# Kernel tuning notes

Measured on AMD Instinct MI355X. Metric: run time of the kernel, lower is better.

## Reference

```python
import jax, jax.numpy as jnp
import numpy as np
from jax import lax

EPS = 1e-5
NUM_HEADS = 8
HEAD_DIM = 64
NUM_DEVICES = 8
MAX_DEV = 3       # max_devices_per_token
TOP_K = 6         # num_experts_per_tok
EBF, DBF, CBF = 0.003, 0.05, 0.02  # aux loss factors


def rms_norm(x, eps=EPS):
    xf = x.astype(jnp.float32)
    var = jnp.mean(jnp.square(xf), axis=-1, keepdims=True)
    return (xf * lax.rsqrt(var + eps)).astype(x.dtype)


def rotate_half(x):
    x1, x2 = jnp.split(x, 2, axis=-1)
    return jnp.concatenate([-x2, x1], axis=-1)


def swiglu(x, wgu, wd):
    gate, up = jnp.split(x @ wgu, 2, axis=-1)
    return (jax.nn.silu(gate) * up) @ wd


def attention(x, w_qkv, w_o, cos, sin):
    B, S, H = x.shape
    qkv = (x @ w_qkv).reshape(B, S, 3 * NUM_HEADS, HEAD_DIM)
    q, k, v = (qkv[:, :, :NUM_HEADS], qkv[:, :, NUM_HEADS:2 * NUM_HEADS],
               qkv[:, :, 2 * NUM_HEADS:])
    c = cos[None, :, None, :]
    s = sin[None, :, None, :]
    q = q * c + rotate_half(q) * s
    k = k * c + rotate_half(k) * s
    scores = jnp.einsum('bqhd,bkhd->bhqk', q, k) / np.float32(np.sqrt(HEAD_DIM))
    p = jax.nn.softmax(scores, axis=-1)  # non-causal
    o = jnp.einsum('bhqk,bkhd->bqhd', p, v).reshape(B, S, H)
    return o @ w_o


def deepseek_moe(x, router_w, r_wgu, r_wd, s_wgu, s_wd):
    B, S, H = x.shape
    E = router_w.shape[1]
    epd = E // NUM_DEVICES
    e2d = jnp.arange(E) // epd  # expert -> device (contiguous blocks)

    logits = x @ router_w                         # [B,S,E]
    probs = jax.nn.softmax(logits, axis=-1)
    # device-limited routing (max_devices_per_token < num_devices)
    dev_scores = probs.reshape(B, S, NUM_DEVICES, epd).sum(-1)  # [B,S,D]
    _, sel_dev = lax.top_k(dev_scores, MAX_DEV)                 # [B,S,3]
    allowed = (sel_dev[..., :, None] == e2d[None, None, None, :]).any(-2)  # [B,S,E]
    masked = jnp.where(allowed, probs, -jnp.inf)
    w, idx = lax.top_k(masked, TOP_K)             # [B,S,K]
    w = jax.nn.softmax(w, axis=-1)

    T = B * S
    xf = x.reshape(T, H)
    idx_f = idx.reshape(T, TOP_K)
    # combine weights [T,E]: scatter-add top-k weights per token
    cw = jnp.zeros((T, E), x.dtype).at[jnp.arange(T)[:, None], idx_f].add(
        w.reshape(T, TOP_K))
    # accumulate weighted expert outputs, streaming one expert at a time
    def body(acc, we):
        wgu, wd, c = we
        return acc + c[:, None] * swiglu(xf, wgu, wd), None
    routed, _ = lax.scan(body, jnp.zeros_like(xf), (r_wgu, r_wd, cw.T))
    routed = routed.reshape(B, S, H)

    shared = swiglu(x, s_wgu[0], s_wd[0]) + swiglu(x, s_wgu[1], s_wd[1])
    out = x + shared + routed

    # auxiliary losses
    f_i = jnp.zeros(E, jnp.float32).at[idx.reshape(-1)].add(1.0) / (T * TOP_K)
    P_i = probs.astype(jnp.float32).mean((0, 1))
    expert_bal = (f_i * P_i).sum() * EBF
    dev_f = f_i.reshape(NUM_DEVICES, epd).mean(-1)
    dev_P = P_i.reshape(NUM_DEVICES, epd).sum(-1)
    device_bal = (dev_f * dev_P).sum() * DBF
    dev_sel = e2d[idx]  # [B,S,K]
    counts = jnp.zeros(NUM_DEVICES, jnp.float32).at[dev_sel.reshape(-1)].add(1.0)
    f_comm = counts / (T * MAX_DEV)
    comm_bal = (f_comm * dev_P).sum() * CBF
    return out, expert_bal, device_bal, comm_bal


def setup_inputs() -> dict:
    key = jax.random.key(0)
    ks = jax.random.split(key, 8)
    B, S, H, E = 4, 1024, 512, 64
    INTER = 1536  # _find_multiple(round(512*4*2/3), 256)
    sc = 1.0 / np.sqrt(H)
    sci = 1.0 / np.sqrt(INTER)
    # RoPE tables
    inv_freq = 1.0 / (10000.0 ** (np.arange(0, HEAD_DIM, 2) / HEAD_DIM))
    freqs = np.outer(np.arange(S), inv_freq)
    emb = np.concatenate([freqs, freqs], axis=-1)
    return {
        'hidden_states': jax.random.normal(ks[0], (B, S, H), jnp.float32),
        'cos': jnp.asarray(np.cos(emb), jnp.float32),
        'sin': jnp.asarray(np.sin(emb), jnp.float32),
        'w_qkv': jax.random.normal(ks[1], (H, 3 * H), jnp.float32) * sc,
        'w_o': jax.random.normal(ks[2], (H, H), jnp.float32) * sc,
        'router_w': jax.random.normal(ks[3], (H, E), jnp.float32) * sc,
        'r_wgu': jax.random.normal(ks[4], (E, H, 2 * INTER), jnp.float32) * sc,
        'r_wd': jax.random.normal(ks[5], (E, INTER, H), jnp.float32) * sci,
        's_wgu': jax.random.normal(ks[6], (2, H, 2 * INTER), jnp.float32) * sc,
        's_wd': jax.random.normal(ks[7], (2, INTER, H), jnp.float32) * sci,
    }


def reference(hidden_states, cos, sin, w_qkv, w_o, router_w, r_wgu, r_wd,
              s_wgu, s_wd):
    h = rms_norm(hidden_states + attention(hidden_states, w_qkv, w_o, cos, sin))
    moe_out, ebl, dbl, cbl = deepseek_moe(h, router_w, r_wgu, r_wd, s_wgu, s_wd)
    h = rms_norm(moe_out)
    return h, ebl, dbl, cbl, ebl + dbl + cbl
```

## Files before the change

### kernel.cpp

```cpp
#include <hip/hip_runtime.h>
#include <math.h>

#define TOK   4096
#define SEQL  1024
#define HID   512
#define NEXP  64
#define FFI   1536
#define NTOPK 6

typedef short bf16x8v __attribute__((ext_vector_type(8)));
typedef float f32x4   __attribute__((ext_vector_type(4)));

__device__ __forceinline__ unsigned short f2bf(float f){
  unsigned int u = __float_as_uint(f);
  u += 0x7fffu + ((u >> 16) & 1u);
  return (unsigned short)(u >> 16);
}
__device__ __forceinline__ float bf2f(unsigned short s){
  return __uint_as_float(((unsigned int)s) << 16);
}

__global__ __launch_bounds__(256) void ktranspose(const float* __restrict__ in,
                                                  float* __restrict__ out, int R, int C){
  __shared__ float tile[32][33];
  int c0 = blockIdx.x * 32, r0 = blockIdx.y * 32;
  int tx = threadIdx.x & 31, ty = threadIdx.x >> 5;
  #pragma unroll
  for (int i = 0; i < 4; i++) tile[ty + i*8][tx] = in[(long long)(r0 + ty + i*8) * C + c0 + tx];
  __syncthreads();
  #pragma unroll
  for (int i = 0; i < 4; i++) out[(long long)(c0 + ty + i*8) * R + r0 + tx] = tile[tx][ty + i*8];
}

__global__ __launch_bounds__(256) void gemm_f32(
    const float* __restrict__ A, const float* __restrict__ B, float* __restrict__ C,
    int K, int lda, int ldb, int ldc, float alpha,
    long long a1, long long a2, int adiv,
    long long b1, long long b2, int bdiv,
    long long c1, long long c2, int cdiv)
{
  int z = blockIdx.z;
  A += (long long)(z / adiv) * a1 + (long long)(z % adiv) * a2;
  B += (long long)(z / bdiv) * b1 + (long long)(z % bdiv) * b2;
  C += (long long)(z / cdiv) * c1 + (long long)(z % cdiv) * c2;
  int m0 = blockIdx.x * 64, n0 = blockIdx.y * 64;
  __shared__ float As[16][68];
  __shared__ float Bs[16][68];
  int tid = threadIdx.x;
  int row = tid >> 2, kq = (tid & 3) * 4;
  int ty = tid >> 4, tx = tid & 15;
  float acc[4][4] = {};
  for (int k0 = 0; k0 < K; k0 += 16){
    float4 av = *(const float4*)&A[(long long)(m0 + row) * lda + k0 + kq];
    float4 bv = *(const float4*)&B[(long long)(n0 + row) * ldb + k0 + kq];
    __syncthreads();
    As[kq+0][row] = av.x; As[kq+1][row] = av.y; As[kq+2][row] = av.z; As[kq+3][row] = av.w;
    Bs[kq+0][row] = bv.x; Bs[kq+1][row] = bv.y; Bs[kq+2][row] = bv.z; Bs[kq+3][row] = bv.w;
    __syncthreads();
    #pragma unroll
    for (int k = 0; k < 16; k++){
      float4 a4 = *(const float4*)&As[k][ty*4];
      float4 b4 = *(const float4*)&Bs[k][tx*4];
      float aa[4] = {a4.x, a4.y, a4.z, a4.w};
      float bb[4] = {b4.x, b4.y, b4.z, b4.w};
      #pragma unroll
      for (int i = 0; i < 4; i++)
        #pragma unroll
        for (int j = 0; j < 4; j++) acc[i][j] += aa[i] * bb[j];
    }
  }
  #pragma unroll
  for (int i = 0; i < 4; i++){
    float4 o;
    o.x = acc[i][0]*alpha; o.y = acc[i][1]*alpha; o.z = acc[i][2]*alpha; o.w = acc[i][3]*alpha;
    *(float4*)&C[(long long)(m0 + ty*4 + i) * ldc + n0 + tx*4] = o;
  }
}

__global__ __launch_bounds__(256) void krope(float* __restrict__ qkv, float* __restrict__ vT,
                                             const float* __restrict__ cosb, const float* __restrict__ sinb){
  int gid = blockIdx.x * 256 + threadIdx.x;
  int t = gid >> 8; int rem = gid & 255; int h = rem >> 5; int d = rem & 31;
  int s = t & (SEQL - 1);
  long long base = (long long)t * 1536 + h * 64;
  float c1 = cosb[s*64 + d], c2 = cosb[s*64 + d + 32];
  float s1 = sinb[s*64 + d], s2 = sinb[s*64 + d + 32];
  float q1 = qkv[base + d], q2 = qkv[base + d + 32];
  qkv[base + d]      = q1*c1 - q2*s1;
  qkv[base + d + 32] = q2*c2 + q1*s2;
  float k1 = qkv[base + 512 + d], k2 = qkv[base + 512 + d + 32];
  qkv[base + 512 + d]      = k1*c1 - k2*s1;
  qkv[base + 512 + d + 32] = k2*c2 + k1*s2;
  float v1 = qkv[base + 1024 + d], v2 = qkv[base + 1024 + d + 32];
  int b = t >> 10;
  long long vb = ((long long)(b*8 + h) * 64) * 1024 + s;
  vT[vb + (long long)d * 1024]        = v1;
  vT[vb + (long long)(d + 32) * 1024] = v2;
}

__global__ __launch_bounds__(256) void ksoftmax(float* __restrict__ sc){
  long long row = blockIdx.x;
  float* p = sc + row * 1024;
  int tid = threadIdx.x;
  float4 v = *(float4*)&p[tid*4];
  float m = fmaxf(fmaxf(v.x, v.y), fmaxf(v.z, v.w));
  for (int o = 32; o > 0; o >>= 1) m = fmaxf(m, __shfl_xor(m, o));
  __shared__ float redm[4], reds[4];
  int wid = tid >> 6, lane = tid & 63;
  if (lane == 0) redm[wid] = m;
  __syncthreads();
  m = fmaxf(fmaxf(redm[0], redm[1]), fmaxf(redm[2], redm[3]));
  float e0 = expf(v.x - m), e1 = expf(v.y - m), e2 = expf(v.z - m), e3 = expf(v.w - m);
  float sum = e0 + e1 + e2 + e3;
  for (int o = 32; o > 0; o >>= 1) sum += __shfl_xor(sum, o);
  if (lane == 0) reds[wid] = sum;
  __syncthreads();
  sum = reds[0] + reds[1] + reds[2] + reds[3];
  float inv = 1.0f / sum;
  float4 o4; o4.x = e0*inv; o4.y = e1*inv; o4.z = e2*inv; o4.w = e3*inv;
  *(float4*)&p[tid*4] = o4;
}

__global__ __launch_bounds__(128) void krms1(const float* __restrict__ x, const float* __restrict__ attn,
    float* __restrict__ h1, unsigned short* __restrict__ h1b, float* __restrict__ macc){
  long long row = blockIdx.x;
  int tid = threadIdx.x;
  float4 xv = *(const float4*)&x[row*512 + tid*4];
  float4 av = *(const float4*)&attn[row*512 + tid*4];
  float4 v; v.x = xv.x+av.x; v.y = xv.y+av.y; v.z = xv.z+av.z; v.w = xv.w+av.w;
  float ss = v.x*v.x + v.y*v.y + v.z*v.z + v.w*v.w;
  for (int o = 32; o > 0; o >>= 1) ss += __shfl_xor(ss, o);
  __shared__ float red[2];
  int wid = tid >> 6, lane = tid & 63;
  if (lane == 0) red[wid] = ss;
  __syncthreads();
  ss = red[0] + red[1];
  float r = 1.0f / sqrtf(ss * (1.0f/512.0f) + 1e-5f);
  float4 o; o.x = v.x*r; o.y = v.y*r; o.z = v.z*r; o.w = v.w*r;
  *(float4*)&h1[row*512 + tid*4] = o;
  *(float4*)&macc[row*512 + tid*4] = o;
  ushort4 ob = make_ushort4(f2bf(o.x), f2bf(o.y), f2bf(o.z), f2bf(o.w));
  *(ushort4*)&h1b[row*512 + tid*4] = ob;
}

__global__ __launch_bounds__(128) void krms2(const float* __restrict__ macc, float* __restrict__ out){
  long long row = blockIdx.x;
  int tid = threadIdx.x;
  float4 v = *(const float4*)&macc[row*512 + tid*4];
  float ss = v.x*v.x + v.y*v.y + v.z*v.z + v.w*v.w;
  for (int o = 32; o > 0; o >>= 1) ss += __shfl_xor(ss, o);
  __shared__ float red[2];
  int wid = tid >> 6, lane = tid & 63;
  if (lane == 0) red[wid] = ss;
  __syncthreads();
  ss = red[0] + red[1];
  float r = 1.0f / sqrtf(ss * (1.0f/512.0f) + 1e-5f);
  float4 o; o.x = v.x*r; o.y = v.y*r; o.z = v.z*r; o.w = v.w*r;
  *(float4*)&out[row*512 + tid*4] = o;
}

__global__ __launch_bounds__(256) void krouter(const float* __restrict__ logits,
    float* __restrict__ probs, int* __restrict__ idx, float* __restrict__ wts, int* __restrict__ cnt){
  int t = blockIdx.x * 4 + (threadIdx.x >> 6);
  int e = threadIdx.x & 63;
  float l = logits[t*64 + e];
  float m = l;
  for (int o = 32; o > 0; o >>= 1) m = fmaxf(m, __shfl_xor(m, o));
  float p = expf(l - m);
  float s = p;
  for (int o = 32; o > 0; o >>= 1) s += __shfl_xor(s, o);
  p /= s;
  probs[t*64 + e] = p;
  float d = p;
  d += __shfl_xor(d, 1); d += __shfl_xor(d, 2); d += __shfl_xor(d, 4);
  int g = e >> 3;
  float mysc = d;
  int rank = 0;
  #pragma unroll
  for (int j = 0; j < 8; j++){
    float sj = __shfl(d, j*8);
    rank += (sj > mysc) || (sj == mysc && j < g);
  }
  float q = (rank < 3) ? p : -INFINITY;
  float svals[6]; int sidx[6];
  #pragma unroll
  for (int kk = 0; kk < 6; kk++){
    float v = q; int vi = e;
    for (int o = 32; o > 0; o >>= 1){
      float ov = __shfl_xor(v, o); int oi = __shfl_xor(vi, o);
      if (ov > v || (ov == v && oi < vi)){ v = ov; vi = oi; }
    }
    svals[kk] = v; sidx[kk] = vi;
    if (e == vi) q = -INFINITY;
  }
  float mx = svals[0], tot = 0.0f, wv[6];
  #pragma unroll
  for (int kk = 0; kk < 6; kk++){ wv[kk] = expf(svals[kk] - mx); tot += wv[kk]; }
  if (e < 6){
    idx[t*6 + e] = sidx[e];
    wts[t*6 + e] = wv[e] / tot;
    atomicAdd(&cnt[sidx[e]], 1);
  }
}

__global__ __launch_bounds__(256) void ksump(const float* __restrict__ probs, float* __restrict__ sumP){
  int e = blockIdx.x; int tid = threadIdx.x;
  float acc = 0.0f;
  for (int t = tid; t < TOK; t += 256) acc += probs[t*64 + e];
  for (int o = 32; o > 0; o >>= 1) acc += __shfl_xor(acc, o);
  __shared__ float red[4];
  int wid = tid >> 6, lane = tid & 63;
  if (lane == 0) red[wid] = acc;
  __syncthreads();
  if (tid == 0) sumP[e] = red[0] + red[1] + red[2] + red[3];
}

__global__ void kfinalize(const int* __restrict__ cnt, int* __restrict__ offs,
                          int2* __restrict__ tiles, int* __restrict__ ntl){
  if (threadIdx.x == 0){
    int acc = 0;
    for (int e = 0; e < 64; e++){ offs[e] = acc; acc += cnt[e]; }
    offs[64] = acc;
    int nt = 0;
    for (int e = 0; e < 64; e++){
      int me = cnt[e];
      for (int m0 = 0; m0 < me; m0 += 128){ tiles[nt] = make_int2(e, m0); nt++; }
    }
    *ntl = nt;
  }
}

__global__ __launch_bounds__(256) void kscatter(const int* __restrict__ idx, const float* __restrict__ wts,
    const int* __restrict__ offs, int* __restrict__ cursor, int* __restrict__ rowsl, float* __restrict__ wrowl){
  int g = blockIdx.x * 256 + threadIdx.x;
  if (g >= TOK * 6) return;
  int t = g / 6, kk = g % 6;
  int e = idx[t*6 + kk];
  int pos = atomicAdd(&cursor[e], 1);
  rowsl[offs[e] + pos] = t;
  wrowl[offs[e] + pos] = wts[t*6 + kk];
}

__global__ __launch_bounds__(256) void kact(const unsigned short* __restrict__ gu,
                                            unsigned short* __restrict__ hact, int total8){
  int g = blockIdx.x * 256 + threadIdx.x;
  if (g >= total8) return;
  int r = g / 192, c8 = (g % 192) * 8;
  const unsigned short* gp = gu + (long long)r * 3072 + c8;
  uint4 gv = *(const uint4*)gp;
  uint4 uv = *(const uint4*)(gp + 1536);
  const unsigned short* gs = (const unsigned short*)&gv;
  const unsigned short* us = (const unsigned short*)&uv;
  unsigned short hv[8] __attribute__((aligned(16)));
  #pragma unroll
  for (int j = 0; j < 8; j++){
    float xg = bf2f(gs[j]);
    float xu = bf2f(us[j]);
    float h = (xg / (1.0f + expf(-xg))) * xu;
    hv[j] = f2bf(h);
  }
  *(uint4*)(hact + (long long)r * 1536 + c8) = *(uint4*)hv;
}

template<int MODE>
__global__ __launch_bounds__(256) void gemm_bf16(
    const unsigned short* __restrict__ Ab, const float* __restrict__ Bb,
    unsigned short* __restrict__ Cb, float* __restrict__ Cacc,
    const int* __restrict__ offs, const int2* __restrict__ tiles, const int* __restrict__ ntl,
    const int* __restrict__ rowsl, const float* __restrict__ wrowl,
    int N, int K)
{
  int e = 0, m0 = 0, roff = 0, Me = 1 << 30;
  long long Boff = 0;
  const unsigned short* A;
  int lda;
  if constexpr (MODE == 0 || MODE == 1){
    if (blockIdx.x >= *ntl) return;
    int2 tl = tiles[blockIdx.x];
    e = tl.x; m0 = tl.y;
    roff = offs[e]; Me = offs[e+1] - roff;
    Boff = (long long)e * K * N;
    if constexpr (MODE == 0){ A = Ab; lda = 512; }
    else { A = Ab + (long long)(roff + m0) * K; lda = K; }
  } else {
    m0 = blockIdx.x * 128;
    int z = blockIdx.z;
    Boff = (long long)z * K * N;
    if constexpr (MODE == 2){ A = Ab; lda = 512; }
    else { A = Ab + (long long)z * 4096 * K; lda = K; }
  }
  const float* B = Bb + Boff;
  int n0 = blockIdx.y * 128;

  __shared__ __align__(16) unsigned short As[128*40];
  __shared__ __align__(16) unsigned short Bs[128*40];

  int tid = threadIdx.x;
  int wid = tid >> 6, lane = tid & 63;
  int wr = wid >> 1, wc = wid & 1;
  int lrow = lane & 15, kgo = (lane >> 4) * 8;

  f32x4 acc[4][4];
  #pragma unroll
  for (int i = 0; i < 4; i++)
    #pragma unroll
    for (int j = 0; j < 4; j++) acc[i][j] = (f32x4){0.f, 0.f, 0.f, 0.f};

  int arow = tid >> 1;
  int acol = (tid & 1) * 16;
  int bn = tid & 127;
  int bkh = (tid >> 7) * 16;

  bool avalid;
  long long asrc;
  if constexpr (MODE == 0){
    avalid = (m0 + arow) < Me;
    int tok = avalid ? rowsl[roff + m0 + arow] : 0;
    asrc = (long long)tok * lda;
  } else if constexpr (MODE == 1){
    avalid = (m0 + arow) < Me;
    asrc = (long long)arow * lda;
  } else {
    avalid = true;
    asrc = (long long)(MODE == 2 ? (m0 + arow) : arow) * lda;
    if constexpr (MODE == 3) asrc = (long long)(m0 + arow) * lda;
  }

  for (int k0 = 0; k0 < K; k0 += 32){
    uint4 a0 = make_uint4(0,0,0,0), a1 = make_uint4(0,0,0,0);
    if (avalid){
      const uint4* ap = (const uint4*)(A + asrc + k0 + acol);
      a0 = ap[0]; a1 = ap[1];
    }
    unsigned short bl[16] __attribute__((aligned(16)));
    const float* bp = B + (long long)(k0 + bkh) * N + n0 + bn;
    #pragma unroll
    for (int j = 0; j < 16; j++) bl[j] = f2bf(bp[(long long)j * N]);
    __syncthreads();
    *(uint4*)&As[arow*40 + acol]     = a0;
    *(uint4*)&As[arow*40 + acol + 8] = a1;
    *(uint4*)&Bs[bn*40 + bkh]        = *(uint4*)&bl[0];
    *(uint4*)&Bs[bn*40 + bkh + 8]    = *(uint4*)&bl[8];
    __syncthreads();
    bf16x8v af[4], bfv[4];
    #pragma unroll
    for (int mi = 0; mi < 4; mi++) af[mi]  = *(const bf16x8v*)&As[(wr*64 + mi*16 + lrow)*40 + kgo];
    #pragma unroll
    for (int nj = 0; nj < 4; nj++) bfv[nj] = *(const bf16x8v*)&Bs[(wc*64 + nj*16 + lrow)*40 + kgo];
    #pragma unroll
    for (int mi = 0; mi < 4; mi++)
      #pragma unroll
      for (int nj = 0; nj < 4; nj++)
        acc[mi][nj] = __builtin_amdgcn_mfma_f32_16x16x32_bf16(af[mi], bfv[nj], acc[mi][nj], 0, 0, 0);
  }

  int crow = wr*64 + (lane >> 4) * 4;
  int ccol = n0 + wc*64 + (lane & 15);
  #pragma unroll
  for (int mi = 0; mi < 4; mi++){
    #pragma unroll
    for (int r = 0; r < 4; r++){
      int lr = crow + mi*16 + r;
      if constexpr (MODE == 0){
        if ((m0 + lr) < Me){
          long long gr = (long long)(roff + m0 + lr);
          #pragma unroll
          for (int nj = 0; nj < 4; nj++)
            Cb[gr * N + ccol + nj*16] = f2bf(acc[mi][nj][r]);
        }
      } else if constexpr (MODE == 1){
        if ((m0 + lr) < Me){
          int gr = roff + m0 + lr;
          int tok = rowsl[gr];
          float wgt = wrowl[gr];
          #pragma unroll
          for (int nj = 0; nj < 4; nj++)
            atomicAdd(&Cacc[(long long)tok * 512 + ccol + nj*16], wgt * acc[mi][nj][r]);
        }
      } else if constexpr (MODE == 2){
        long long gr = (long long)blockIdx.z * 4096 + m0 + lr;
        #pragma unroll
        for (int nj = 0; nj < 4; nj++)
          Cb[gr * N + ccol + nj*16] = f2bf(acc[mi][nj][r]);
      } else {
        #pragma unroll
        for (int nj = 0; nj < 4; nj++)
          atomicAdd(&Cacc[(long long)(m0 + lr) * 512 + ccol + nj*16], acc[mi][nj][r]);
      }
    }
  }
}

__global__ void kscalars(const int* __restrict__ cnt, const float* __restrict__ sumP, float* __restrict__ o){
  int e = threadIdx.x;
  float cf = (float)cnt[e];
  float f = cf / 24576.0f;
  float P = sumP[e] / 4096.0f;
  float fg = f, Pg = P, cg = cf;
  fg += __shfl_xor(fg, 1); fg += __shfl_xor(fg, 2); fg += __shfl_xor(fg, 4);
  Pg += __shfl_xor(Pg, 1); Pg += __shfl_xor(Pg, 2); Pg += __shfl_xor(Pg, 4);
  cg += __shfl_xor(cg, 1); cg += __shfl_xor(cg, 2); cg += __shfl_xor(cg, 4);
  float t1 = f * P;
  float t2 = ((e & 7) == 0) ? (fg / 8.0f) * Pg : 0.0f;
  float t3 = ((e & 7) == 0) ? (cg / 12288.0f) * Pg : 0.0f;
  for (int s = 32; s > 0; s >>= 1){
    t1 += __shfl_xor(t1, s); t2 += __shfl_xor(t2, s); t3 += __shfl_xor(t3, s);
  }
  if (e == 0){
    float ebl = t1 * 0.003f, dbl = t2 * 0.05f, cbl = t3 * 0.02f;
    o[0] = ebl; o[1] = dbl; o[2] = cbl; o[3] = ebl + dbl + cbl;
  }
}

extern "C" void kernel_launch(void* const* d_in, const int* in_sizes, int n_in,
                              void* d_out, int out_size, void* d_ws, size_t ws_size,
                              hipStream_t stream){
  const float* x        = (const float*)d_in[0];
  const float* cosb     = (const float*)d_in[1];
  const float* sinb     = (const float*)d_in[2];
  const float* w_qkv    = (const float*)d_in[3];
  const float* w_o      = (const float*)d_in[4];
  const float* router_w = (const float*)d_in[5];
  const float* r_wgu    = (const float*)d_in[6];
  const float* r_wd     = (const float*)d_in[7];
  const float* s_wgu    = (const float*)d_in[8];
  const float* s_wd     = (const float*)d_in[9];
  float* out = (float*)d_out;

  char* wsp = (char*)d_ws;
  auto alloc = [&](size_t bytes)->char*{
    char* p = wsp; wsp += (bytes + 255) & ~(size_t)255; return p;
  };
  float* qkv   = (float*)alloc(4096ULL*1536*4);
  float* vT    = (float*)alloc(32ULL*64*1024*4);
  float* wqkvT = (float*)alloc(1536ULL*512*4);
  float* woT   = (float*)alloc(512ULL*512*4);
  float* wrT   = (float*)alloc(64ULL*512*4);
  float* attno = (float*)alloc(4096ULL*512*4);
  float* attnw = (float*)alloc(4096ULL*512*4);
  float* h1    = (float*)alloc(4096ULL*512*4);
  unsigned short* h1b = (unsigned short*)alloc(4096ULL*512*2);
  float* macc  = (float*)alloc(4096ULL*512*4);
  float* logits= (float*)alloc(4096ULL*64*4);
  float* probs = (float*)alloc(4096ULL*64*4);
  int*   idx   = (int*)alloc(4096ULL*6*4);
  float* wts   = (float*)alloc(4096ULL*6*4);
  int*   cnt   = (int*)alloc(64*4);
  int*   cursor= (int*)alloc(64*4);
  int*   offs  = (int*)alloc(65*4);
  int*   ntl   = (int*)alloc(256);
  float* sumP  = (float*)alloc(64*4);
  int2*  tiles = (int2*)alloc(512*8);
  int*   rowsl = (int*)alloc(24576ULL*4);
  float* wrowl = (float*)alloc(24576ULL*4);
  char* region = alloc(24576ULL*3072*2 + 24576ULL*1536*2 + 2ULL*4096*3072*2 + 2ULL*4096*1536*2);
  float* scores = (float*)region;
  unsigned short* gu    = (unsigned short*)region;
  unsigned short* hact  = (unsigned short*)(region + 24576ULL*3072*2);
  unsigned short* sgu   = (unsigned short*)(region + 24576ULL*3072*2 + 24576ULL*1536*2);
  unsigned short* shact = (unsigned short*)(region + 24576ULL*3072*2 + 24576ULL*1536*2 + 2ULL*4096*3072*2);

  hipMemsetAsync(cnt, 0, 512, stream);

  ktranspose<<<dim3(48, 16), 256, 0, stream>>>(w_qkv, wqkvT, 512, 1536);
  ktranspose<<<dim3(16, 16), 256, 0, stream>>>(w_o, woT, 512, 512);
  ktranspose<<<dim3(2, 16),  256, 0, stream>>>(router_w, wrT, 512, 64);

  gemm_f32<<<dim3(64, 24, 1), 256, 0, stream>>>(x, wqkvT, qkv, 512, 512, 512, 1536, 1.0f,
      0,0,1, 0,0,1, 0,0,1);
  krope<<<4096, 256, 0, stream>>>(qkv, vT, cosb, sinb);
  gemm_f32<<<dim3(16, 16, 32), 256, 0, stream>>>(qkv, qkv + 512, scores, 64, 1536, 1536, 1024, 0.125f,
      (long long)1024*1536, 64, 8,
      (long long)1024*1536, 64, 8,
      (long long)1024*1024, 0, 1);
  ksoftmax<<<32768, 256, 0, stream>>>(scores);
  gemm_f32<<<dim3(16, 1, 32), 256, 0, stream>>>(scores, vT, attno, 1024, 1024, 1024, 512, 1.0f,
      (long long)1024*1024, 0, 1,
      (long long)64*1024, 0, 1,
      (long long)1024*512, 64, 8);
  gemm_f32<<<dim3(64, 8, 1), 256, 0, stream>>>(attno, woT, attnw, 512, 512, 512, 512, 1.0f,
      0,0,1, 0,0,1, 0,0,1);
  krms1<<<4096, 128, 0, stream>>>(x, attnw, h1, h1b, macc);
  gemm_f32<<<dim3(64, 1, 1), 256, 0, stream>>>(h1, wrT, logits, 512, 512, 512, 64, 1.0f,
      0,0,1, 0,0,1, 0,0,1);
  krouter<<<1024, 256, 0, stream>>>(logits, probs, idx, wts, cnt);
  ksump<<<64, 256, 0, stream>>>(probs, sumP);
  kfinalize<<<1, 64, 0, stream>>>(cnt, offs, tiles, ntl);
  kscatter<<<96, 256, 0, stream>>>(idx, wts, offs, cursor, rowsl, wrowl);

  gemm_bf16<0><<<dim3(256, 24, 1), 256, 0, stream>>>(h1b, r_wgu, gu, nullptr,
      offs, tiles, ntl, rowsl, wrowl, 3072, 512);
  gemm_bf16<2><<<dim3(32, 24, 2), 256, 0, stream>>>(h1b, s_wgu, sgu, nullptr,
      offs, tiles, ntl, rowsl, wrowl, 3072, 512);
  kact<<<(24576*192 + 255)/256, 256, 0, stream>>>(gu, hact, 24576*192);
  kact<<<(8192*192 + 255)/256, 256, 0, stream>>>(sgu, shact, 8192*192);
  gemm_bf16<1><<<dim3(256, 4, 1), 256, 0, stream>>>(hact, r_wd, nullptr, macc,
      offs, tiles, ntl, rowsl, wrowl, 512, 1536);
  gemm_bf16<3><<<dim3(32, 4, 2), 256, 0, stream>>>(shact, s_wd, nullptr, macc,
      offs, tiles, ntl, rowsl, wrowl, 512, 1536);

  krms2<<<4096, 128, 0, stream>>>(macc, out);
  kscalars<<<1, 64, 0, stream>>>(cnt, sumP, out + 4096ULL*512);
}
```

Measured before the change: 1.103 ms.

## Replace FP32 SIMT GEMMs with split-bf16 MFMA GEMMs and restructure MoE pipeline

All dense fp32 GEMMs (QKV, attention scores, PV, output projection, router) now run on bf16 MFMA using a three-product hi/lo split to keep near-fp32 accuracy. Inputs, weights, softmax outputs and V are pre-split into hi/lo bf16 planes by new conversion kernels. The MoE path gets pre-transposed, pre-converted expert weights with gate/up interleaving so activation fuses into the first FFN GEMM, and routing adds a near-tie fix-up kernel. This trades extra conversion passes and memory traffic for much higher matrix throughput, but converts large expert weights on every call.

```diff
diff --git a/kernel.cpp b/kernel.cpp
--- a/kernel.cpp
+++ b/kernel.cpp
@@ -6,7 +6,6 @@
 #define HID   512
 #define NEXP  64
 #define FFI   1536
-#define NTOPK 6
 
 typedef short bf16x8v __attribute__((ext_vector_type(8)));
 typedef float f32x4   __attribute__((ext_vector_type(4)));
@@ -19,128 +18,265 @@
 __device__ __forceinline__ float bf2f(unsigned short s){
   return __uint_as_float(((unsigned int)s) << 16);
 }
-
-__global__ __launch_bounds__(256) void ktranspose(const float* __restrict__ in,
-                                                  float* __restrict__ out, int R, int C){
-  __shared__ float tile[32][33];
-  int c0 = blockIdx.x * 32, r0 = blockIdx.y * 32;
-  int tx = threadIdx.x & 31, ty = threadIdx.x >> 5;
-  #pragma unroll
-  for (int i = 0; i < 4; i++) tile[ty + i*8][tx] = in[(long long)(r0 + ty + i*8) * C + c0 + tx];
-  __syncthreads();
-  #pragma unroll
-  for (int i = 0; i < 4; i++) out[(long long)(c0 + ty + i*8) * R + r0 + tx] = tile[tx][ty + i*8];
-}
-
-__global__ __launch_bounds__(256) void gemm_f32(
-    const float* __restrict__ A, const float* __restrict__ B, float* __restrict__ C,
-    int K, int lda, int ldb, int ldc, float alpha,
+__device__ __forceinline__ void split2(float v, unsigned short& h, unsigned short& l){
+  h = f2bf(v);
+  l = f2bf(v - bf2f(h));
+}
+
+__global__ __launch_bounds__(256) void ksplit(const float* __restrict__ in,
+    unsigned short* __restrict__ hi, unsigned short* __restrict__ lo, int n4){
+  int g = blockIdx.x*256 + threadIdx.x;
+  if (g >= n4) return;
+  float4 v = *(const float4*)&in[(long long)g*4];
+  unsigned short h0,h1,h2,h3,l0,l1,l2,l3;
+  split2(v.x,h0,l0); split2(v.y,h1,l1); split2(v.z,h2,l2); split2(v.w,h3,l3);
+  *(ushort4*)&hi[(long long)g*4] = make_ushort4(h0,h1,h2,h3);
+  *(ushort4*)&lo[(long long)g*4] = make_ushort4(l0,l1,l2,l3);
+}
+
+__global__ __launch_bounds__(256) void kTsplit(const float* __restrict__ in,
+    unsigned short* __restrict__ ohi, unsigned short* __restrict__ olo, int R, int C){
+  __shared__ float tile[64][65];
+  int c0 = blockIdx.x*64, r0 = blockIdx.y*64;
+  int tid = threadIdx.x;
+  #pragma unroll
+  for (int it=0; it<4; it++){
+    int idx = it*256+tid; int r = idx>>4; int cq = (idx&15)*4;
+    float4 v = *(const float4*)&in[(long long)(r0+r)*C + c0 + cq];
+    tile[r][cq]=v.x; tile[r][cq+1]=v.y; tile[r][cq+2]=v.z; tile[r][cq+3]=v.w;
+  }
+  __syncthreads();
+  #pragma unroll
+  for (int it=0; it<2; it++){
+    int idx = it*256+tid; int c = idx>>3; int rq=(idx&7)*8;
+    unsigned short th[8] __attribute__((aligned(16)));
+    unsigned short tl[8] __attribute__((aligned(16)));
+    #pragma unroll
+    for (int j=0;j<8;j++){
+      float f = tile[rq+j][c];
+      split2(f, th[j], tl[j]);
+    }
+    long long o = (long long)(c0+c)*R + r0 + rq;
+    *(uint4*)&ohi[o] = *(uint4*)th;
+    *(uint4*)&olo[o] = *(uint4*)tl;
+  }
+}
+
+template<bool PAIRED>
+__global__ __launch_bounds__(256) void kconvT(const float* __restrict__ in,
+    unsigned short* __restrict__ out, int R, int C){
+  __shared__ float tile[64][65];
+  long long zb = (long long)blockIdx.z * R * C;
+  int c0 = blockIdx.x*64, r0 = blockIdx.y*64;
+  int tid = threadIdx.x;
+  #pragma unroll
+  for (int it=0; it<4; it++){
+    int idx = it*256+tid; int r = idx>>4; int cq = (idx&15)*4;
+    float4 v = *(const float4*)&in[zb + (long long)(r0+r)*C + c0 + cq];
+    tile[r][cq]=v.x; tile[r][cq+1]=v.y; tile[r][cq+2]=v.z; tile[r][cq+3]=v.w;
+  }
+  __syncthreads();
+  #pragma unroll
+  for (int it=0; it<2; it++){
+    int idx = it*256+tid; int c = idx>>3; int rq=(idx&7)*8;
+    unsigned short tb[8] __attribute__((aligned(16)));
+    #pragma unroll
+    for (int j=0;j<8;j++) tb[j] = f2bf(tile[rq+j][c]);
+    int cc = c0 + c;
+    int orow = PAIRED ? ((cc < (C>>1)) ? 2*cc : 2*(cc-(C>>1))+1) : cc;
+    *(uint4*)&out[zb + (long long)orow*R + r0 + rq] = *(uint4*)tb;
+  }
+}
+
+template<int WM,int WN,int FM,int FN>
+__global__ __launch_bounds__(256) void gemm_x3(
+    const unsigned short* __restrict__ Ahi, const unsigned short* __restrict__ Alo,
+    const unsigned short* __restrict__ Bhi, const unsigned short* __restrict__ Blo,
+    float* __restrict__ C, int K, int lda, int ldb, int ldc, float alpha,
     long long a1, long long a2, int adiv,
     long long b1, long long b2, int bdiv,
     long long c1, long long c2, int cdiv)
 {
+  constexpr int BM = WM*FM*16, BN = WN*FN*16;
+  constexpr int AIT = (2*BM*4)/256, BIT = (2*BN*4)/256;
   int z = blockIdx.z;
-  A += (long long)(z / adiv) * a1 + (long long)(z % adiv) * a2;
-  B += (long long)(z / bdiv) * b1 + (long long)(z % bdiv) * b2;
-  C += (long long)(z / cdiv) * c1 + (long long)(z % cdiv) * c2;
-  int m0 = blockIdx.x * 64, n0 = blockIdx.y * 64;
-  __shared__ float As[16][68];
-  __shared__ float Bs[16][68];
+  long long aoff = (long long)(z/adiv)*a1 + (long long)(z%adiv)*a2;
+  long long boff = (long long)(z/bdiv)*b1 + (long long)(z%bdiv)*b2;
+  C += (long long)(z/cdiv)*c1 + (long long)(z%cdiv)*c2;
+  int m0 = blockIdx.x*BM, n0 = blockIdx.y*BN;
+  __shared__ __align__(16) unsigned short As[2][BM*40];
+  __shared__ __align__(16) unsigned short Bs[2][BN*40];
+  int tid = threadIdx.x, lane = tid&63, wid = tid>>6;
+  int wr = wid / WN, wc = wid % WN;
+  int lrow = lane&15, kgo = (lane>>4)*8;
+  f32x4 acc[FM][FN];
+  #pragma unroll
+  for (int mi=0;mi<FM;mi++)
+    #pragma unroll
+    for (int nj=0;nj<FN;nj++) acc[mi][nj] = (f32x4){0.f,0.f,0.f,0.f};
+
+  for (int k0=0; k0<K; k0+=32){
+    uint4 ta[AIT], tb[BIT];
+    #pragma unroll
+    for (int it=0; it<AIT; it++){
+      int c = it*256+tid; int pl = c/(BM*4); int rem = c%(BM*4);
+      int row = rem>>2, q = (rem&3)*8;
+      const unsigned short* src = pl ? Alo : Ahi;
+      ta[it] = *(const uint4*)&src[aoff + (long long)(m0+row)*lda + k0 + q];
+    }
+    #pragma unroll
+    for (int it=0; it<BIT; it++){
+      int c = it*256+tid; int pl = c/(BN*4); int rem = c%(BN*4);
+      int row = rem>>2, q = (rem&3)*8;
+      const unsigned short* src = pl ? Blo : Bhi;
+      tb[it] = *(const uint4*)&src[boff + (long long)(n0+row)*ldb + k0 + q];
+    }
+    __syncthreads();
+    #pragma unroll
+    for (int it=0; it<AIT; it++){
+      int c = it*256+tid; int pl = c/(BM*4); int rem = c%(BM*4);
+      int row = rem>>2, q = (rem&3)*8;
+      *(uint4*)&As[pl][row*40+q] = ta[it];
+    }
+    #pragma unroll
+    for (int it=0; it<BIT; it++){
+      int c = it*256+tid; int pl = c/(BN*4); int rem = c%(BN*4);
+      int row = rem>>2, q = (rem&3)*8;
+      *(uint4*)&Bs[pl][row*40+q] = tb[it];
+    }
+    __syncthreads();
+    bf16x8v ah[FM], al[FM], bh[FN], bl[FN];
+    int ab = (wr*FM*16 + lrow)*40 + kgo;
+    int bb = (wc*FN*16 + lrow)*40 + kgo;
+    #pragma unroll
+    for (int mi=0;mi<FM;mi++){
+      ah[mi] = *(const bf16x8v*)&As[0][ab + mi*640];
+      al[mi] = *(const bf16x8v*)&As[1][ab + mi*640];
+    }
+    #pragma unroll
+    for (int nj=0;nj<FN;nj++){
+      bh[nj] = *(const bf16x8v*)&Bs[0][bb + nj*640];
+      bl[nj] = *(const bf16x8v*)&Bs[1][bb + nj*640];
+    }
+    #pragma unroll
+    for (int mi=0;mi<FM;mi++)
+      #pragma unroll
+      for (int nj=0;nj<FN;nj++){
+        acc[mi][nj] = __builtin_amdgcn_mfma_f32_16x16x32_bf16(ah[mi], bh[nj], acc[mi][nj], 0,0,0);
+        acc[mi][nj] = __builtin_amdgcn_mfma_f32_16x16x32_bf16(ah[mi], bl[nj], acc[mi][nj], 0,0,0);
+        acc[mi][nj] = __builtin_amdgcn_mfma_f32_16x16x32_bf16(al[mi], bh[nj], acc[mi][nj], 0,0,0);
+      }
+  }
+  int crow = m0 + wr*FM*16 + ((lane>>4)<<2);
+  int ccol = n0 + wc*FN*16 + (lane&15);
+  #pragma unroll
+  for (int mi=0;mi<FM;mi++)
+    #pragma unroll
+    for (int r=0;r<4;r++){
+      long long row = crow + mi*16 + r;
+      #pragma unroll
+      for (int nj=0;nj<FN;nj++)
+        C[row*ldc + ccol + nj*16] = alpha*acc[mi][nj][r];
+    }
+}
+
+__global__ __launch_bounds__(256) void krope(float* __restrict__ qkv,
+    unsigned short* __restrict__ qhi, unsigned short* __restrict__ qlo,
+    const float* __restrict__ cosb, const float* __restrict__ sinb){
+  int gid = blockIdx.x*256 + threadIdx.x;
+  int t = gid >> 8; int rem = gid & 255; int h = rem >> 5; int d = rem & 31;
+  int s = t & (SEQL-1);
+  long long base = (long long)t*1536 + h*64;
+  float c1 = cosb[s*64+d], c2 = cosb[s*64+d+32];
+  float s1 = sinb[s*64+d], s2 = sinb[s*64+d+32];
+  float q1 = qkv[base+d], q2 = qkv[base+d+32];
+  float rq1 = q1*c1 - q2*s1, rq2 = q2*c2 + q1*s2;
+  qkv[base+d] = rq1; qkv[base+d+32] = rq2;
+  split2(rq1, qhi[base+d],    qlo[base+d]);
+  split2(rq2, qhi[base+d+32], qlo[base+d+32]);
+  float k1 = qkv[base+512+d], k2 = qkv[base+512+d+32];
+  float rk1 = k1*c1 - k2*s1, rk2 = k2*c2 + k1*s2;
+  qkv[base+512+d] = rk1; qkv[base+512+d+32] = rk2;
+  split2(rk1, qhi[base+512+d],    qlo[base+512+d]);
+  split2(rk2, qhi[base+512+d+32], qlo[base+512+d+32]);
+}
+
+__global__ __launch_bounds__(256) void kvtrans(const float* __restrict__ qkv,
+    unsigned short* __restrict__ vhi, unsigned short* __restrict__ vlo){
+  __shared__ float tile[64][65];
+  int s0 = blockIdx.x*64;
+  int z = blockIdx.y;
+  int b = z >> 3, h = z & 7;
   int tid = threadIdx.x;
-  int row = tid >> 2, kq = (tid & 3) * 4;
-  int ty = tid >> 4, tx = tid & 15;
-  float acc[4][4] = {};
-  for (int k0 = 0; k0 < K; k0 += 16){
-    float4 av = *(const float4*)&A[(long long)(m0 + row) * lda + k0 + kq];
-    float4 bv = *(const float4*)&B[(long long)(n0 + row) * ldb + k0 + kq];
-    __syncthreads();
-    As[kq+0][row] = av.x; As[kq+1][row] = av.y; As[kq+2][row] = av.z; As[kq+3][row] = av.w;
-    Bs[kq+0][row] = bv.x; Bs[kq+1][row] = bv.y; Bs[kq+2][row] = bv.z; Bs[kq+3][row] = bv.w;
-    __syncthreads();
-    #pragma unroll
-    for (int k = 0; k < 16; k++){
-      float4 a4 = *(const float4*)&As[k][ty*4];
-      float4 b4 = *(const float4*)&Bs[k][tx*4];
-      float aa[4] = {a4.x, a4.y, a4.z, a4.w};
-      float bb[4] = {b4.x, b4.y, b4.z, b4.w};
-      #pragma unroll
-      for (int i = 0; i < 4; i++)
-        #pragma unroll
-        for (int j = 0; j < 4; j++) acc[i][j] += aa[i] * bb[j];
-    }
-  }
-  #pragma unroll
-  for (int i = 0; i < 4; i++){
-    float4 o;
-    o.x = acc[i][0]*alpha; o.y = acc[i][1]*alpha; o.z = acc[i][2]*alpha; o.w = acc[i][3]*alpha;
-    *(float4*)&C[(long long)(m0 + ty*4 + i) * ldc + n0 + tx*4] = o;
-  }
-}
-
-__global__ __launch_bounds__(256) void krope(float* __restrict__ qkv, float* __restrict__ vT,
-                                             const float* __restrict__ cosb, const float* __restrict__ sinb){
-  int gid = blockIdx.x * 256 + threadIdx.x;
-  int t = gid >> 8; int rem = gid & 255; int h = rem >> 5; int d = rem & 31;
-  int s = t & (SEQL - 1);
-  long long base = (long long)t * 1536 + h * 64;
-  float c1 = cosb[s*64 + d], c2 = cosb[s*64 + d + 32];
-  float s1 = sinb[s*64 + d], s2 = sinb[s*64 + d + 32];
-  float q1 = qkv[base + d], q2 = qkv[base + d + 32];
-  qkv[base + d]      = q1*c1 - q2*s1;
-  qkv[base + d + 32] = q2*c2 + q1*s2;
-  float k1 = qkv[base + 512 + d], k2 = qkv[base + 512 + d + 32];
-  qkv[base + 512 + d]      = k1*c1 - k2*s1;
-  qkv[base + 512 + d + 32] = k2*c2 + k1*s2;
-  float v1 = qkv[base + 1024 + d], v2 = qkv[base + 1024 + d + 32];
-  int b = t >> 10;
-  long long vb = ((long long)(b*8 + h) * 64) * 1024 + s;
-  vT[vb + (long long)d * 1024]        = v1;
-  vT[vb + (long long)(d + 32) * 1024] = v2;
-}
-
-__global__ __launch_bounds__(256) void ksoftmax(float* __restrict__ sc){
+  #pragma unroll
+  for (int it=0; it<4; it++){
+    int idx = it*256+tid; int r = idx>>4; int cq = (idx&15)*4;
+    float4 v = *(const float4*)&qkv[((long long)(b*1024 + s0 + r))*1536 + 1024 + h*64 + cq];
+    tile[r][cq]=v.x; tile[r][cq+1]=v.y; tile[r][cq+2]=v.z; tile[r][cq+3]=v.w;
+  }
+  __syncthreads();
+  #pragma unroll
+  for (int it=0; it<2; it++){
+    int idx = it*256+tid; int d = idx>>3; int sq = (idx&7)*8;
+    unsigned short th[8] __attribute__((aligned(16)));
+    unsigned short tl[8] __attribute__((aligned(16)));
+    #pragma unroll
+    for (int j=0;j<8;j++) split2(tile[sq+j][d], th[j], tl[j]);
+    long long o = ((long long)(z*64 + d))*1024 + s0 + sq;
+    *(uint4*)&vhi[o] = *(uint4*)th;
+    *(uint4*)&vlo[o] = *(uint4*)tl;
+  }
+}
+
+__global__ __launch_bounds__(256) void ksoftmax(const float* __restrict__ sc,
+    unsigned short* __restrict__ phi, unsigned short* __restrict__ plo){
   long long row = blockIdx.x;
-  float* p = sc + row * 1024;
+  const float* p = sc + row*1024;
   int tid = threadIdx.x;
-  float4 v = *(float4*)&p[tid*4];
-  float m = fmaxf(fmaxf(v.x, v.y), fmaxf(v.z, v.w));
-  for (int o = 32; o > 0; o >>= 1) m = fmaxf(m, __shfl_xor(m, o));
+  float4 v = *(const float4*)&p[tid*4];
+  float m = fmaxf(fmaxf(v.x,v.y), fmaxf(v.z,v.w));
+  for (int o=32;o>0;o>>=1) m = fmaxf(m, __shfl_xor(m,o));
   __shared__ float redm[4], reds[4];
-  int wid = tid >> 6, lane = tid & 63;
-  if (lane == 0) redm[wid] = m;
-  __syncthreads();
-  m = fmaxf(fmaxf(redm[0], redm[1]), fmaxf(redm[2], redm[3]));
-  float e0 = expf(v.x - m), e1 = expf(v.y - m), e2 = expf(v.z - m), e3 = expf(v.w - m);
-  float sum = e0 + e1 + e2 + e3;
-  for (int o = 32; o > 0; o >>= 1) sum += __shfl_xor(sum, o);
-  if (lane == 0) reds[wid] = sum;
-  __syncthreads();
-  sum = reds[0] + reds[1] + reds[2] + reds[3];
-  float inv = 1.0f / sum;
-  float4 o4; o4.x = e0*inv; o4.y = e1*inv; o4.z = e2*inv; o4.w = e3*inv;
-  *(float4*)&p[tid*4] = o4;
+  int wid = tid>>6, lane = tid&63;
+  if (lane==0) redm[wid]=m;
+  __syncthreads();
+  m = fmaxf(fmaxf(redm[0],redm[1]), fmaxf(redm[2],redm[3]));
+  float e0=expf(v.x-m), e1=expf(v.y-m), e2=expf(v.z-m), e3=expf(v.w-m);
+  float sum = e0+e1+e2+e3;
+  for (int o=32;o>0;o>>=1) sum += __shfl_xor(sum,o);
+  if (lane==0) reds[wid]=sum;
+  __syncthreads();
+  sum = reds[0]+reds[1]+reds[2]+reds[3];
+  float inv = 1.0f/sum;
+  unsigned short h0,h1,h2,h3,l0,l1,l2,l3;
+  split2(e0*inv,h0,l0); split2(e1*inv,h1,l1); split2(e2*inv,h2,l2); split2(e3*inv,h3,l3);
+  *(ushort4*)&phi[row*1024 + tid*4] = make_ushort4(h0,h1,h2,h3);
+  *(ushort4*)&plo[row*1024 + tid*4] = make_ushort4(l0,l1,l2,l3);
 }
 
 __global__ __launch_bounds__(128) void krms1(const float* __restrict__ x, const float* __restrict__ attn,
-    float* __restrict__ h1, unsigned short* __restrict__ h1b, float* __restrict__ macc){
+    unsigned short* __restrict__ h1hi, unsigned short* __restrict__ h1lo,
+    unsigned short* __restrict__ h1b, float* __restrict__ macc){
   long long row = blockIdx.x;
   int tid = threadIdx.x;
   float4 xv = *(const float4*)&x[row*512 + tid*4];
   float4 av = *(const float4*)&attn[row*512 + tid*4];
-  float4 v; v.x = xv.x+av.x; v.y = xv.y+av.y; v.z = xv.z+av.z; v.w = xv.w+av.w;
+  float4 v; v.x=xv.x+av.x; v.y=xv.y+av.y; v.z=xv.z+av.z; v.w=xv.w+av.w;
   float ss = v.x*v.x + v.y*v.y + v.z*v.z + v.w*v.w;
-  for (int o = 32; o > 0; o >>= 1) ss += __shfl_xor(ss, o);
+  for (int o=32;o>0;o>>=1) ss += __shfl_xor(ss,o);
   __shared__ float red[2];
-  int wid = tid >> 6, lane = tid & 63;
-  if (lane == 0) red[wid] = ss;
-  __syncthreads();
-  ss = red[0] + red[1];
-  float r = 1.0f / sqrtf(ss * (1.0f/512.0f) + 1e-5f);
-  float4 o; o.x = v.x*r; o.y = v.y*r; o.z = v.z*r; o.w = v.w*r;
-  *(float4*)&h1[row*512 + tid*4] = o;
+  int wid = tid>>6, lane = tid&63;
+  if (lane==0) red[wid]=ss;
+  __syncthreads();
+  ss = red[0]+red[1];
+  float r = 1.0f/sqrtf(ss*(1.0f/512.0f) + 1e-5f);
+  float4 o; o.x=v.x*r; o.y=v.y*r; o.z=v.z*r; o.w=v.w*r;
   *(float4*)&macc[row*512 + tid*4] = o;
-  ushort4 ob = make_ushort4(f2bf(o.x), f2bf(o.y), f2bf(o.z), f2bf(o.w));
-  *(ushort4*)&h1b[row*512 + tid*4] = ob;
+  unsigned short h0,h1,h2,h3,l0,l1,l2,l3;
+  split2(o.x,h0,l0); split2(o.y,h1,l1); split2(o.z,h2,l2); split2(o.w,h3,l3);
+  *(ushort4*)&h1hi[row*512 + tid*4] = make_ushort4(h0,h1,h2,h3);
+  *(ushort4*)&h1lo[row*512 + tid*4] = make_ushort4(l0,l1,l2,l3);
+  *(ushort4*)&h1b[row*512 + tid*4] = make_ushort4(f2bf(o.x),f2bf(o.y),f2bf(o.z),f2bf(o.w));
 }
 
 __global__ __launch_bounds__(128) void krms2(const float* __restrict__ macc, float* __restrict__ out){
@@ -148,83 +284,201 @@
   int tid = threadIdx.x;
   float4 v = *(const float4*)&macc[row*512 + tid*4];
   float ss = v.x*v.x + v.y*v.y + v.z*v.z + v.w*v.w;
-  for (int o = 32; o > 0; o >>= 1) ss += __shfl_xor(ss, o);
+  for (int o=32;o>0;o>>=1) ss += __shfl_xor(ss,o);
   __shared__ float red[2];
-  int wid = tid >> 6, lane = tid & 63;
-  if (lane == 0) red[wid] = ss;
-  __syncthreads();
-  ss = red[0] + red[1];
-  float r = 1.0f / sqrtf(ss * (1.0f/512.0f) + 1e-5f);
-  float4 o; o.x = v.x*r; o.y = v.y*r; o.z = v.z*r; o.w = v.w*r;
+  int wid = tid>>6, lane = tid&63;
+  if (lane==0) red[wid]=ss;
+  __syncthreads();
+  ss = red[0]+red[1];
+  float r = 1.0f/sqrtf(ss*(1.0f/512.0f) + 1e-5f);
+  float4 o; o.x=v.x*r; o.y=v.y*r; o.z=v.z*r; o.w=v.w*r;
   *(float4*)&out[row*512 + tid*4] = o;
 }
 
+__device__ void route_decide(float p, int e, int t,
+    int* __restrict__ idx, float* __restrict__ wts,
+    int* __restrict__ flagcnt, int* __restrict__ flaglist){
+  float d = p;
+  d += __shfl_xor(d,1); d += __shfl_xor(d,2); d += __shfl_xor(d,4);
+  int g = e >> 3;
+  float gs[8];
+  #pragma unroll
+  for (int j=0;j<8;j++) gs[j] = __shfl(d, j*8);
+  int rank = 0;
+  #pragma unroll
+  for (int j=0;j<8;j++) rank += (gs[j] > d) || (gs[j] == d && j < g);
+  float q = (rank < 3) ? p : -INFINITY;
+  float svals[7]; int sidx[7];
+  #pragma unroll
+  for (int kk=0; kk<7; kk++){
+    float v = q; int vi = e;
+    for (int o=32;o>0;o>>=1){
+      float ov = __shfl_xor(v,o); int oi = __shfl_xor(vi,o);
+      if (ov > v || (ov == v && oi < vi)){ v = ov; vi = oi; }
+    }
+    svals[kk] = v; sidx[kk] = vi;
+    if (e == vi) q = -INFINITY;
+  }
+  float mx = svals[0], tot = 0.f, wv[6];
+  #pragma unroll
+  for (int kk=0;kk<6;kk++){ wv[kk] = expf(svals[kk]-mx); tot += wv[kk]; }
+  if (e < 6){
+    idx[t*6+e] = sidx[e];
+    wts[t*6+e] = wv[e]/tot;
+  }
+  if (flagcnt != nullptr && e == 0){
+    float a[8];
+    #pragma unroll
+    for (int j=0;j<8;j++) a[j] = gs[j];
+    float t3=-1e30f, t4=-1e30f;
+    for (int it2=0; it2<4; it2++){
+      int bi=0; float bv=a[0];
+      #pragma unroll
+      for (int j=1;j<8;j++) if (a[j] > bv){ bv=a[j]; bi=j; }
+      if (it2==2) t3=bv;
+      if (it2==3) t4=bv;
+      a[bi] = -1e30f;
+    }
+    float pgap = svals[5] - svals[6];
+    float dgap = t3 - t4;
+    if (pgap < 1e-4f || dgap < 5e-4f){
+      int pos = atomicAdd(flagcnt, 1);
+      if (pos < 1024) flaglist[pos] = t;
+    }
+  }
+}
+
 __global__ __launch_bounds__(256) void krouter(const float* __restrict__ logits,
-    float* __restrict__ probs, int* __restrict__ idx, float* __restrict__ wts, int* __restrict__ cnt){
-  int t = blockIdx.x * 4 + (threadIdx.x >> 6);
+    float* __restrict__ probs, int* __restrict__ idx, float* __restrict__ wts,
+    int* __restrict__ flagcnt, int* __restrict__ flaglist){
+  int t = blockIdx.x*4 + (threadIdx.x >> 6);
   int e = threadIdx.x & 63;
   float l = logits[t*64 + e];
   float m = l;
-  for (int o = 32; o > 0; o >>= 1) m = fmaxf(m, __shfl_xor(m, o));
-  float p = expf(l - m);
+  for (int o=32;o>0;o>>=1) m = fmaxf(m, __shfl_xor(m,o));
+  float p = expf(l-m);
   float s = p;
-  for (int o = 32; o > 0; o >>= 1) s += __shfl_xor(s, o);
+  for (int o=32;o>0;o>>=1) s += __shfl_xor(s,o);
   p /= s;
-  probs[t*64 + e] = p;
-  float d = p;
-  d += __shfl_xor(d, 1); d += __shfl_xor(d, 2); d += __shfl_xor(d, 4);
-  int g = e >> 3;
-  float mysc = d;
-  int rank = 0;
-  #pragma unroll
-  for (int j = 0; j < 8; j++){
-    float sj = __shfl(d, j*8);
-    rank += (sj > mysc) || (sj == mysc && j < g);
-  }
-  float q = (rank < 3) ? p : -INFINITY;
-  float svals[6]; int sidx[6];
-  #pragma unroll
-  for (int kk = 0; kk < 6; kk++){
-    float v = q; int vi = e;
-    for (int o = 32; o > 0; o >>= 1){
-      float ov = __shfl_xor(v, o); int oi = __shfl_xor(vi, o);
-      if (ov > v || (ov == v && oi < vi)){ v = ov; vi = oi; }
-    }
-    svals[kk] = v; sidx[kk] = vi;
-    if (e == vi) q = -INFINITY;
-  }
-  float mx = svals[0], tot = 0.0f, wv[6];
-  #pragma unroll
-  for (int kk = 0; kk < 6; kk++){ wv[kk] = expf(svals[kk] - mx); tot += wv[kk]; }
-  if (e < 6){
-    idx[t*6 + e] = sidx[e];
-    wts[t*6 + e] = wv[e] / tot;
-    atomicAdd(&cnt[sidx[e]], 1);
-  }
+  probs[t*64+e] = p;
+  route_decide(p, e, t, idx, wts, flagcnt, flaglist);
+}
+
+__global__ __launch_bounds__(256) void kfix(const int* __restrict__ flagcnt, const int* __restrict__ flaglist,
+    const float* __restrict__ qkv, const float* __restrict__ x,
+    const float* __restrict__ w_o, const float* __restrict__ router_w,
+    int* __restrict__ idx, float* __restrict__ wts, float* __restrict__ probs){
+  int fc = *flagcnt; if (fc > 1024) fc = 1024;
+  if ((int)blockIdx.x >= fc) return;
+  int t = flaglist[blockIdx.x];
+  int b = t >> 10;
+  int tid = threadIdx.x;
+  __shared__ float sc[1024];
+  __shared__ float qh[64];
+  __shared__ float o512[512];
+  __shared__ float h1s[512];
+  __shared__ float op[4][64];
+  __shared__ float red[4];
+  const float* qrow = qkv + (long long)t*1536;
+  const float* kbase = qkv + (long long)b*1024*1536;
+  for (int h=0; h<8; h++){
+    if (tid < 64) qh[tid] = qrow[h*64 + tid];
+    __syncthreads();
+    for (int s = tid; s < 1024; s += 256){
+      const float* kr = kbase + (long long)s*1536 + 512 + h*64;
+      float a0 = 0.f;
+      #pragma unroll 8
+      for (int d2=0; d2<64; d2++) a0 += qh[d2]*kr[d2];
+      sc[s] = a0 * 0.125f;
+    }
+    __syncthreads();
+    float m = -1e30f;
+    for (int s=tid; s<1024; s+=256) m = fmaxf(m, sc[s]);
+    #pragma unroll
+    for (int o=32;o>0;o>>=1) m = fmaxf(m, __shfl_xor(m,o));
+    if ((tid&63)==0) red[tid>>6]=m;
+    __syncthreads();
+    m = fmaxf(fmaxf(red[0],red[1]), fmaxf(red[2],red[3]));
+    __syncthreads();
+    float sum = 0.f;
+    for (int s=tid; s<1024; s+=256){ float e2 = expf(sc[s]-m); sc[s]=e2; sum += e2; }
+    #pragma unroll
+    for (int o=32;o>0;o>>=1) sum += __shfl_xor(sum,o);
+    if ((tid&63)==0) red[tid>>6]=sum;
+    __syncthreads();
+    sum = red[0]+red[1]+red[2]+red[3];
+    float inv = 1.0f/sum;
+    int d2 = tid & 63, ch = tid >> 6;
+    float a1 = 0.f;
+    const float* vb = kbase + 1024 + h*64 + d2;
+    for (int s=ch*256; s<ch*256+256; s++) a1 += sc[s]*vb[(long long)s*1536];
+    op[ch][d2] = a1;
+    __syncthreads();
+    if (tid < 64) o512[h*64+tid] = (op[0][tid]+op[1][tid]+op[2][tid]+op[3][tid])*inv;
+    __syncthreads();
+  }
+  int j0 = tid, j1 = tid+256;
+  float a0 = 0.f, a1 = 0.f;
+  for (int i=0;i<512;i++){
+    float oi = o512[i];
+    a0 += oi*w_o[(long long)i*512 + j0];
+    a1 += oi*w_o[(long long)i*512 + j1];
+  }
+  float hj0 = x[(long long)t*512 + j0] + a0;
+  float hj1 = x[(long long)t*512 + j1] + a1;
+  float ss = hj0*hj0 + hj1*hj1;
+  #pragma unroll
+  for (int o=32;o>0;o>>=1) ss += __shfl_xor(ss,o);
+  __syncthreads();
+  if ((tid&63)==0) red[tid>>6]=ss;
+  __syncthreads();
+  ss = red[0]+red[1]+red[2]+red[3];
+  float r = 1.0f/sqrtf(ss*(1.0f/512.0f) + 1e-5f);
+  h1s[j0] = hj0*r; h1s[j1] = hj1*r;
+  __syncthreads();
+  if (tid < 64){
+    int e = tid;
+    float le = 0.f;
+    for (int i=0;i<512;i++) le += h1s[i]*router_w[(long long)i*64 + e];
+    float m2 = le;
+    #pragma unroll
+    for (int o=32;o>0;o>>=1) m2 = fmaxf(m2, __shfl_xor(m2,o));
+    float p = expf(le - m2), s2 = p;
+    #pragma unroll
+    for (int o=32;o>0;o>>=1) s2 += __shfl_xor(s2,o);
+    p /= s2;
+    probs[(long long)t*64 + e] = p;
+    route_decide(p, e, t, idx, wts, nullptr, nullptr);
+  }
+}
+
+__global__ void kcount(const int* __restrict__ idx, int* __restrict__ cnt){
+  int g = blockIdx.x*256 + threadIdx.x;
+  if (g < TOK*6) atomicAdd(&cnt[idx[g]], 1);
 }
 
 __global__ __launch_bounds__(256) void ksump(const float* __restrict__ probs, float* __restrict__ sumP){
   int e = blockIdx.x; int tid = threadIdx.x;
-  float acc = 0.0f;
+  float acc = 0.f;
   for (int t = tid; t < TOK; t += 256) acc += probs[t*64 + e];
-  for (int o = 32; o > 0; o >>= 1) acc += __shfl_xor(acc, o);
+  for (int o=32;o>0;o>>=1) acc += __shfl_xor(acc,o);
   __shared__ float red[4];
-  int wid = tid >> 6, lane = tid & 63;
-  if (lane == 0) red[wid] = acc;
-  __syncthreads();
-  if (tid == 0) sumP[e] = red[0] + red[1] + red[2] + red[3];
+  int wid = tid>>6, lane = tid&63;
+  if (lane==0) red[wid]=acc;
+  __syncthreads();
+  if (tid==0) sumP[e] = red[0]+red[1]+red[2]+red[3];
 }
 
 __global__ void kfinalize(const int* __restrict__ cnt, int* __restrict__ offs,
                           int2* __restrict__ tiles, int* __restrict__ ntl){
   if (threadIdx.x == 0){
     int acc = 0;
-    for (int e = 0; e < 64; e++){ offs[e] = acc; acc += cnt[e]; }
-    offs[64] = acc;
+    for (int e=0;e<64;e++){ offs[e]=acc; acc += cnt[e]; }
+    offs[64]=acc;
     int nt = 0;
-    for (int e = 0; e < 64; e++){
+    for (int e=0;e<64;e++){
       int me = cnt[e];
-      for (int m0 = 0; m0 < me; m0 += 128){ tiles[nt] = make_int2(e, m0); nt++; }
+      for (int m0=0;m0<me;m0+=128){ tiles[nt] = make_int2(e,m0); nt++; }
     }
     *ntl = nt;
   }
@@ -232,162 +486,141 @@
 
 __global__ __launch_bounds__(256) void kscatter(const int* __restrict__ idx, const float* __restrict__ wts,
     const int* __restrict__ offs, int* __restrict__ cursor, int* __restrict__ rowsl, float* __restrict__ wrowl){
-  int g = blockIdx.x * 256 + threadIdx.x;
-  if (g >= TOK * 6) return;
-  int t = g / 6, kk = g % 6;
-  int e = idx[t*6 + kk];
+  int g = blockIdx.x*256 + threadIdx.x;
+  if (g >= TOK*6) return;
+  int t = g/6, kk = g%6;
+  int e = idx[t*6+kk];
   int pos = atomicAdd(&cursor[e], 1);
-  rowsl[offs[e] + pos] = t;
-  wrowl[offs[e] + pos] = wts[t*6 + kk];
-}
-
-__global__ __launch_bounds__(256) void kact(const unsigned short* __restrict__ gu,
-                                            unsigned short* __restrict__ hact, int total8){
-  int g = blockIdx.x * 256 + threadIdx.x;
-  if (g >= total8) return;
-  int r = g / 192, c8 = (g % 192) * 8;
-  const unsigned short* gp = gu + (long long)r * 3072 + c8;
-  uint4 gv = *(const uint4*)gp;
-  uint4 uv = *(const uint4*)(gp + 1536);
-  const unsigned short* gs = (const unsigned short*)&gv;
-  const unsigned short* us = (const unsigned short*)&uv;
-  unsigned short hv[8] __attribute__((aligned(16)));
-  #pragma unroll
-  for (int j = 0; j < 8; j++){
-    float xg = bf2f(gs[j]);
-    float xu = bf2f(us[j]);
-    float h = (xg / (1.0f + expf(-xg))) * xu;
-    hv[j] = f2bf(h);
-  }
-  *(uint4*)(hact + (long long)r * 1536 + c8) = *(uint4*)hv;
+  rowsl[offs[e]+pos] = t;
+  wrowl[offs[e]+pos] = wts[t*6+kk];
 }
 
 template<int MODE>
-__global__ __launch_bounds__(256) void gemm_bf16(
-    const unsigned short* __restrict__ Ab, const float* __restrict__ Bb,
-    unsigned short* __restrict__ Cb, float* __restrict__ Cacc,
+__global__ __launch_bounds__(256) void gemm_ffn(
+    const unsigned short* __restrict__ Ab, const unsigned short* __restrict__ Bw,
+    unsigned short* __restrict__ Cact, float* __restrict__ macc,
     const int* __restrict__ offs, const int2* __restrict__ tiles, const int* __restrict__ ntl,
     const int* __restrict__ rowsl, const float* __restrict__ wrowl,
     int N, int K)
 {
-  int e = 0, m0 = 0, roff = 0, Me = 1 << 30;
-  long long Boff = 0;
-  const unsigned short* A;
-  int lda;
-  if constexpr (MODE == 0 || MODE == 1){
-    if (blockIdx.x >= *ntl) return;
+  int e=0, m0=0, roff=0, Me=1<<30;
+  long long Aoff=0, Boff=0;
+  int zi = blockIdx.z;
+  if constexpr (MODE==0 || MODE==1){
+    if ((int)blockIdx.x >= *ntl) return;
     int2 tl = tiles[blockIdx.x];
     e = tl.x; m0 = tl.y;
-    roff = offs[e]; Me = offs[e+1] - roff;
-    Boff = (long long)e * K * N;
-    if constexpr (MODE == 0){ A = Ab; lda = 512; }
-    else { A = Ab + (long long)(roff + m0) * K; lda = K; }
+    roff = offs[e]; Me = offs[e+1]-roff;
+    Boff = (long long)e*N*K;
+    if constexpr (MODE==1) Aoff = (long long)roff*K;
   } else {
-    m0 = blockIdx.x * 128;
-    int z = blockIdx.z;
-    Boff = (long long)z * K * N;
-    if constexpr (MODE == 2){ A = Ab; lda = 512; }
-    else { A = Ab + (long long)z * 4096 * K; lda = K; }
-  }
-  const float* B = Bb + Boff;
-  int n0 = blockIdx.y * 128;
-
+    m0 = blockIdx.x*128;
+    Boff = (long long)zi*N*K;
+    if constexpr (MODE==3) Aoff = (long long)zi*4096*K;
+  }
+  int n0 = blockIdx.y*128;
   __shared__ __align__(16) unsigned short As[128*40];
   __shared__ __align__(16) unsigned short Bs[128*40];
-
-  int tid = threadIdx.x;
-  int wid = tid >> 6, lane = tid & 63;
-  int wr = wid >> 1, wc = wid & 1;
-  int lrow = lane & 15, kgo = (lane >> 4) * 8;
-
+  int tid = threadIdx.x, lane = tid&63, wid = tid>>6;
+  int wr = wid>>1, wc = wid&1;
+  int lrow = lane&15, kgo = (lane>>4)*8;
   f32x4 acc[4][4];
   #pragma unroll
-  for (int i = 0; i < 4; i++)
-    #pragma unroll
-    for (int j = 0; j < 4; j++) acc[i][j] = (f32x4){0.f, 0.f, 0.f, 0.f};
-
-  int arow = tid >> 1;
-  int acol = (tid & 1) * 16;
-  int bn = tid & 127;
-  int bkh = (tid >> 7) * 16;
-
-  bool avalid;
-  long long asrc;
-  if constexpr (MODE == 0){
-    avalid = (m0 + arow) < Me;
-    int tok = avalid ? rowsl[roff + m0 + arow] : 0;
-    asrc = (long long)tok * lda;
-  } else if constexpr (MODE == 1){
-    avalid = (m0 + arow) < Me;
-    asrc = (long long)arow * lda;
-  } else {
-    avalid = true;
-    asrc = (long long)(MODE == 2 ? (m0 + arow) : arow) * lda;
-    if constexpr (MODE == 3) asrc = (long long)(m0 + arow) * lda;
-  }
-
-  for (int k0 = 0; k0 < K; k0 += 32){
-    uint4 a0 = make_uint4(0,0,0,0), a1 = make_uint4(0,0,0,0);
-    if (avalid){
-      const uint4* ap = (const uint4*)(A + asrc + k0 + acol);
-      a0 = ap[0]; a1 = ap[1];
-    }
-    unsigned short bl[16] __attribute__((aligned(16)));
-    const float* bp = B + (long long)(k0 + bkh) * N + n0 + bn;
-    #pragma unroll
-    for (int j = 0; j < 16; j++) bl[j] = f2bf(bp[(long long)j * N]);
-    __syncthreads();
-    *(uint4*)&As[arow*40 + acol]     = a0;
-    *(uint4*)&As[arow*40 + acol + 8] = a1;
-    *(uint4*)&Bs[bn*40 + bkh]        = *(uint4*)&bl[0];
-    *(uint4*)&Bs[bn*40 + bkh + 8]    = *(uint4*)&bl[8];
-    __syncthreads();
-    bf16x8v af[4], bfv[4];
-    #pragma unroll
-    for (int mi = 0; mi < 4; mi++) af[mi]  = *(const bf16x8v*)&As[(wr*64 + mi*16 + lrow)*40 + kgo];
-    #pragma unroll
-    for (int nj = 0; nj < 4; nj++) bfv[nj] = *(const bf16x8v*)&Bs[(wc*64 + nj*16 + lrow)*40 + kgo];
-    #pragma unroll
-    for (int mi = 0; mi < 4; mi++)
+  for (int mi=0;mi<4;mi++)
+    #pragma unroll
+    for (int nj=0;nj<4;nj++) acc[mi][nj] = (f32x4){0.f,0.f,0.f,0.f};
+
+  for (int k0=0; k0<K; k0+=32){
+    uint4 ta[2], tb[2];
+    #pragma unroll
+    for (int it=0;it<2;it++){
+      int c = it*256+tid; int row=c>>2; int q=(c&3)*8;
+      long long asrc;
+      if constexpr (MODE==0){
+        bool valid = (m0+row) < Me;
+        int tok = valid ? rowsl[roff+m0+row] : 0;
+        asrc = (long long)tok*512;
+      } else if constexpr (MODE==2){
+        asrc = (long long)(m0+row)*512;
+      } else {
+        asrc = Aoff + (long long)(m0+row)*(long long)K;
+      }
+      ta[it] = *(const uint4*)&Ab[asrc + k0 + q];
+      tb[it] = *(const uint4*)&Bw[Boff + (long long)(n0+row)*K + k0 + q];
+    }
+    __syncthreads();
+    #pragma unroll
+    for (int it=0;it<2;it++){
+      int c = it*256+tid; int row=c>>2; int q=(c&3)*8;
+      *(uint4*)&As[row*40+q] = ta[it];
+      *(uint4*)&Bs[row*40+q] = tb[it];
+    }
+    __syncthreads();
+    bf16x8v af[4], bf[4];
+    int ab = (wr*64 + lrow)*40 + kgo;
+    int bb = (wc*64 + lrow)*40 + kgo;
+    #pragma unroll
+    for (int mi=0;mi<4;mi++) af[mi] = *(const bf16x8v*)&As[ab + mi*640];
+    #pragma unroll
+    for (int nj=0;nj<4;nj++) bf[nj] = *(const bf16x8v*)&Bs[bb + nj*640];
+    #pragma unroll
+    for (int mi=0;mi<4;mi++)
       #pragma unroll
-      for (int nj = 0; nj < 4; nj++)
-        acc[mi][nj] = __builtin_amdgcn_mfma_f32_16x16x32_bf16(af[mi], bfv[nj], acc[mi][nj], 0, 0, 0);
-  }
-
-  int crow = wr*64 + (lane >> 4) * 4;
-  int ccol = n0 + wc*64 + (lane & 15);
-  #pragma unroll
-  for (int mi = 0; mi < 4; mi++){
-    #pragma unroll
-    for (int r = 0; r < 4; r++){
-      int lr = crow + mi*16 + r;
-      if constexpr (MODE == 0){
-        if ((m0 + lr) < Me){
-          long long gr = (long long)(roff + m0 + lr);
-          #pragma unroll
-          for (int nj = 0; nj < 4; nj++)
-            Cb[gr * N + ccol + nj*16] = f2bf(acc[mi][nj][r]);
+      for (int nj=0;nj<4;nj++)
+        acc[mi][nj] = __builtin_amdgcn_mfma_f32_16x16x32_bf16(af[mi], bf[nj], acc[mi][nj], 0,0,0);
+  }
+
+  int crow = wr*64 + ((lane>>4)<<2);
+  int ccol = wc*64 + (lane&15);
+  if constexpr (MODE==0 || MODE==2){
+    bool evenlane = (lane&1)==0;
+    #pragma unroll
+    for (int mi=0;mi<4;mi++){
+      #pragma unroll
+      for (int r2=0;r2<4;r2++){
+        int lr = crow + mi*16 + r2;
+        bool valid; long long grow;
+        if constexpr (MODE==0){ valid = (m0+lr)<Me; grow = roff+m0+lr; }
+        else { valid = true; grow = (long long)zi*4096 + m0 + lr; }
+        #pragma unroll
+        for (int nj=0;nj<4;nj++){
+          float v = acc[mi][nj][r2];
+          float o2 = __shfl_xor(v,1);
+          float g = evenlane ? v : o2;
+          float u = evenlane ? o2 : v;
+          float sg = g/(1.0f+expf(-g))*u;
+          if (evenlane && valid){
+            int col = n0 + ccol + nj*16;
+            Cact[grow*1536 + (col>>1)] = f2bf(sg);
+          }
         }
-      } else if constexpr (MODE == 1){
-        if ((m0 + lr) < Me){
-          int gr = roff + m0 + lr;
+      }
+    }
+  } else if constexpr (MODE==1){
+    #pragma unroll
+    for (int mi=0;mi<4;mi++)
+      #pragma unroll
+      for (int r2=0;r2<4;r2++){
+        int lr = crow + mi*16 + r2;
+        if ((m0+lr) < Me){
+          int gr = roff+m0+lr;
           int tok = rowsl[gr];
           float wgt = wrowl[gr];
           #pragma unroll
-          for (int nj = 0; nj < 4; nj++)
-            atomicAdd(&Cacc[(long long)tok * 512 + ccol + nj*16], wgt * acc[mi][nj][r]);
+          for (int nj=0;nj<4;nj++)
+            atomicAdd(&macc[(long long)tok*512 + n0 + ccol + nj*16], wgt*acc[mi][nj][r2]);
         }
-      } else if constexpr (MODE == 2){
-        long long gr = (long long)blockIdx.z * 4096 + m0 + lr;
+      }
+  } else {
+    #pragma unroll
+    for (int mi=0;mi<4;mi++)
+      #pragma unroll
+      for (int r2=0;r2<4;r2++){
+        long long tok = m0 + crow + mi*16 + r2;
         #pragma unroll
-        for (int nj = 0; nj < 4; nj++)
-          Cb[gr * N + ccol + nj*16] = f2bf(acc[mi][nj][r]);
-      } else {
-        #pragma unroll
-        for (int nj = 0; nj < 4; nj++)
-          atomicAdd(&Cacc[(long long)(m0 + lr) * 512 + ccol + nj*16], acc[mi][nj][r]);
+        for (int nj=0;nj<4;nj++)
+          atomicAdd(&macc[tok*512 + n0 + ccol + nj*16], acc[mi][nj][r2]);
       }
-    }
   }
 }
 
@@ -397,18 +630,18 @@
   float f = cf / 24576.0f;
   float P = sumP[e] / 4096.0f;
   float fg = f, Pg = P, cg = cf;
-  fg += __shfl_xor(fg, 1); fg += __shfl_xor(fg, 2); fg += __shfl_xor(fg, 4);
-  Pg += __shfl_xor(Pg, 1); Pg += __shfl_xor(Pg, 2); Pg += __shfl_xor(Pg, 4);
-  cg += __shfl_xor(cg, 1); cg += __shfl_xor(cg, 2); cg += __shfl_xor(cg, 4);
-  float t1 = f * P;
-  float t2 = ((e & 7) == 0) ? (fg / 8.0f) * Pg : 0.0f;
-  float t3 = ((e & 7) == 0) ? (cg / 12288.0f) * Pg : 0.0f;
-  for (int s = 32; s > 0; s >>= 1){
-    t1 += __shfl_xor(t1, s); t2 += __shfl_xor(t2, s); t3 += __shfl_xor(t3, s);
-  }
-  if (e == 0){
-    float ebl = t1 * 0.003f, dbl = t2 * 0.05f, cbl = t3 * 0.02f;
-    o[0] = ebl; o[1] = dbl; o[2] = cbl; o[3] = ebl + dbl + cbl;
+  fg += __shfl_xor(fg,1); fg += __shfl_xor(fg,2); fg += __shfl_xor(fg,4);
+  Pg += __shfl_xor(Pg,1); Pg += __shfl_xor(Pg,2); Pg += __shfl_xor(Pg,4);
+  cg += __shfl_xor(cg,1); cg += __shfl_xor(cg,2); cg += __shfl_xor(cg,4);
+  float t1 = f*P;
+  float t2 = ((e&7)==0) ? (fg/8.0f)*Pg : 0.0f;
+  float t3 = ((e&7)==0) ? (cg/12288.0f)*Pg : 0.0f;
+  for (int s=32;s>0;s>>=1){
+    t1 += __shfl_xor(t1,s); t2 += __shfl_xor(t2,s); t3 += __shfl_xor(t3,s);
+  }
+  if (e==0){
+    float ebl = t1*0.003f, dbl = t2*0.05f, cbl = t3*0.02f;
+    o[0]=ebl; o[1]=dbl; o[2]=cbl; o[3]=ebl+dbl+cbl;
   }
 }
 
@@ -427,78 +660,115 @@
   const float* s_wd     = (const float*)d_in[9];
   float* out = (float*)d_out;
 
-  char* wsp = (char*)d_ws;
-  auto alloc = [&](size_t bytes)->char*{
-    char* p = wsp; wsp += (bytes + 255) & ~(size_t)255; return p;
+  char* base = (char*)d_ws;
+  size_t off = 0;
+  auto alloc = [&](size_t b)->char*{
+    char* p = base + off; off = (off + b + 255) & ~(size_t)255; return p;
   };
-  float* qkv   = (float*)alloc(4096ULL*1536*4);
-  float* vT    = (float*)alloc(32ULL*64*1024*4);
-  float* wqkvT = (float*)alloc(1536ULL*512*4);
-  float* woT   = (float*)alloc(512ULL*512*4);
-  float* wrT   = (float*)alloc(64ULL*512*4);
-  float* attno = (float*)alloc(4096ULL*512*4);
-  float* attnw = (float*)alloc(4096ULL*512*4);
-  float* h1    = (float*)alloc(4096ULL*512*4);
-  unsigned short* h1b = (unsigned short*)alloc(4096ULL*512*2);
-  float* macc  = (float*)alloc(4096ULL*512*4);
-  float* logits= (float*)alloc(4096ULL*64*4);
-  float* probs = (float*)alloc(4096ULL*64*4);
-  int*   idx   = (int*)alloc(4096ULL*6*4);
-  float* wts   = (float*)alloc(4096ULL*6*4);
-  int*   cnt   = (int*)alloc(64*4);
-  int*   cursor= (int*)alloc(64*4);
-  int*   offs  = (int*)alloc(65*4);
-  int*   ntl   = (int*)alloc(256);
-  float* sumP  = (float*)alloc(64*4);
-  int2*  tiles = (int2*)alloc(512*8);
-  int*   rowsl = (int*)alloc(24576ULL*4);
-  float* wrowl = (float*)alloc(24576ULL*4);
-  char* region = alloc(24576ULL*3072*2 + 24576ULL*1536*2 + 2ULL*4096*3072*2 + 2ULL*4096*1536*2);
-  float* scores = (float*)region;
-  unsigned short* gu    = (unsigned short*)region;
-  unsigned short* hact  = (unsigned short*)(region + 24576ULL*3072*2);
-  unsigned short* sgu   = (unsigned short*)(region + 24576ULL*3072*2 + 24576ULL*1536*2);
-  unsigned short* shact = (unsigned short*)(region + 24576ULL*3072*2 + 24576ULL*1536*2 + 2ULL*4096*3072*2);
-
-  hipMemsetAsync(cnt, 0, 512, stream);
-
-  ktranspose<<<dim3(48, 16), 256, 0, stream>>>(w_qkv, wqkvT, 512, 1536);
-  ktranspose<<<dim3(16, 16), 256, 0, stream>>>(w_o, woT, 512, 512);
-  ktranspose<<<dim3(2, 16),  256, 0, stream>>>(router_w, wrT, 512, 64);
-
-  gemm_f32<<<dim3(64, 24, 1), 256, 0, stream>>>(x, wqkvT, qkv, 512, 512, 512, 1536, 1.0f,
-      0,0,1, 0,0,1, 0,0,1);
-  krope<<<4096, 256, 0, stream>>>(qkv, vT, cosb, sinb);
-  gemm_f32<<<dim3(16, 16, 32), 256, 0, stream>>>(qkv, qkv + 512, scores, 64, 1536, 1536, 1024, 0.125f,
-      (long long)1024*1536, 64, 8,
-      (long long)1024*1536, 64, 8,
-      (long long)1024*1024, 0, 1);
-  ksoftmax<<<32768, 256, 0, stream>>>(scores);
-  gemm_f32<<<dim3(16, 1, 32), 256, 0, stream>>>(scores, vT, attno, 1024, 1024, 1024, 512, 1.0f,
-      (long long)1024*1024, 0, 1,
-      (long long)64*1024, 0, 1,
-      (long long)1024*512, 64, 8);
-  gemm_f32<<<dim3(64, 8, 1), 256, 0, stream>>>(attno, woT, attnw, 512, 512, 512, 512, 1.0f,
-      0,0,1, 0,0,1, 0,0,1);
-  krms1<<<4096, 128, 0, stream>>>(x, attnw, h1, h1b, macc);
-  gemm_f32<<<dim3(64, 1, 1), 256, 0, stream>>>(h1, wrT, logits, 512, 512, 512, 64, 1.0f,
-      0,0,1, 0,0,1, 0,0,1);
-  krouter<<<1024, 256, 0, stream>>>(logits, probs, idx, wts, cnt);
+  unsigned short* x_hi   = (unsigned short*)alloc(2097152ULL*2);
+  unsigned short* x_lo   = (unsigned short*)alloc(2097152ULL*2);
+  unsigned short* wqkvT_hi = (unsigned short*)alloc(786432ULL*2);
+  unsigned short* wqkvT_lo = (unsigned short*)alloc(786432ULL*2);
+  unsigned short* woT_hi = (unsigned short*)alloc(262144ULL*2);
+  unsigned short* woT_lo = (unsigned short*)alloc(262144ULL*2);
+  unsigned short* wrT_hi = (unsigned short*)alloc(32768ULL*2);
+  unsigned short* wrT_lo = (unsigned short*)alloc(32768ULL*2);
+  unsigned short* h1_hi  = (unsigned short*)alloc(2097152ULL*2);
+  unsigned short* h1_lo  = (unsigned short*)alloc(2097152ULL*2);
+  unsigned short* h1b    = (unsigned short*)alloc(2097152ULL*2);
+  float* macc   = (float*)alloc(2097152ULL*4);
+  float* logits = (float*)alloc(262144ULL*4);
+  float* probs  = (float*)alloc(262144ULL*4);
+  int*   idx    = (int*)alloc(24576ULL*4);
+  float* wts    = (float*)alloc(24576ULL*4);
+  int*   cnt     = (int*)alloc(256);
+  int*   cursor  = (int*)alloc(256);
+  int*   flagcnt = (int*)alloc(256);
+  int*   flaglist= (int*)alloc(1024*4);
+  int*   offs   = (int*)alloc(65*4);
+  int*   ntl    = (int*)alloc(256);
+  float* sumP   = (float*)alloc(64*4);
+  int2*  tiles  = (int2*)alloc(512*8);
+  int*   rowsl  = (int*)alloc(24576ULL*4);
+  float* wrowl  = (float*)alloc(24576ULL*4);
+
+  size_t region = off;
+  size_t oA = region, oF = region;
+  auto allocV = [&](size_t b, size_t& o2)->char*{
+    char* p = base + o2; o2 = (o2 + b + 255) & ~(size_t)255; return p;
+  };
+  float* qkv    = (float*)allocV(6291456ULL*4, oA);
+  unsigned short* qkv_hi = (unsigned short*)allocV(6291456ULL*2, oA);
+  unsigned short* qkv_lo = (unsigned short*)allocV(6291456ULL*2, oA);
+  unsigned short* vT_hi  = (unsigned short*)allocV(2097152ULL*2, oA);
+  unsigned short* vT_lo  = (unsigned short*)allocV(2097152ULL*2, oA);
+  float* scores = (float*)allocV(8388608ULL*4, oA);
+  unsigned short* p_hi = (unsigned short*)allocV(16777216ULL*2, oA);
+  unsigned short* p_lo = (unsigned short*)allocV(16777216ULL*2, oA);
+  float* attno = (float*)allocV(2097152ULL*4, oA);
+  unsigned short* attno_hi = (unsigned short*)allocV(2097152ULL*2, oA);
+  unsigned short* attno_lo = (unsigned short*)allocV(2097152ULL*2, oA);
+  float* attnw = (float*)allocV(2097152ULL*4, oA);
+  unsigned short* wguT = (unsigned short*)allocV(100663296ULL*2, oF);
+  unsigned short* sguT = (unsigned short*)allocV(3145728ULL*2, oF);
+  unsigned short* hact = (unsigned short*)allocV(37748736ULL*2, oF);
+  unsigned short* shact= (unsigned short*)allocV(12582912ULL*2, oF);
+  unsigned short* wdT  = wguT;
+  unsigned short* swdT = wguT + 50331648ULL;
+
+  hipMemsetAsync(cnt, 0, 768, stream);
+
+  ksplit<<<2048, 256, 0, stream>>>(x, x_hi, x_lo, 524288);
+  kTsplit<<<dim3(24,8), 256, 0, stream>>>(w_qkv, wqkvT_hi, wqkvT_lo, 512, 1536);
+  kTsplit<<<dim3(8,8),  256, 0, stream>>>(w_o, woT_hi, woT_lo, 512, 512);
+  kTsplit<<<dim3(1,8),  256, 0, stream>>>(router_w, wrT_hi, wrT_lo, 512, 64);
+
+  gemm_x3<2,2,4,4><<<dim3(32,12,1), 256, 0, stream>>>(x_hi, x_lo, wqkvT_hi, wqkvT_lo,
+      qkv, 512, 512, 512, 1536, 1.0f, 0,0,1, 0,0,1, 0,0,1);
+  krope<<<4096, 256, 0, stream>>>(qkv, qkv_hi, qkv_lo, cosb, sinb);
+  kvtrans<<<dim3(16,32), 256, 0, stream>>>(qkv, vT_hi, vT_lo);
+
+  for (int bp = 0; bp < 2; bp++){
+    for (int lb = 0; lb < 2; lb++){
+      int b = bp*2 + lb;
+      const unsigned short* qa = qkv_hi + (size_t)b*1572864;
+      const unsigned short* ql = qkv_lo + (size_t)b*1572864;
+      gemm_x3<2,2,4,4><<<dim3(8,8,8), 256, 0, stream>>>(qa, ql, qa+512, ql+512,
+          scores, 64, 1536, 1536, 1024, 0.125f, 0,64,8, 0,64,8, 0,1048576LL,8);
+      ksoftmax<<<8192, 256, 0, stream>>>(scores,
+          p_hi + (size_t)lb*8388608, p_lo + (size_t)lb*8388608);
+    }
+    gemm_x3<2,2,2,2><<<dim3(16,1,16), 256, 0, stream>>>(p_hi, p_lo,
+        vT_hi + (size_t)bp*1048576, vT_lo + (size_t)bp*1048576,
+        attno + (size_t)bp*1048576, 1024, 1024, 1024, 512, 1.0f,
+        1048576LL,0,1, 65536LL,0,1, 524288LL,64,8);
+  }
+  ksplit<<<2048, 256, 0, stream>>>(attno, attno_hi, attno_lo, 524288);
+  gemm_x3<2,2,4,4><<<dim3(32,4,1), 256, 0, stream>>>(attno_hi, attno_lo, woT_hi, woT_lo,
+      attnw, 512, 512, 512, 512, 1.0f, 0,0,1, 0,0,1, 0,0,1);
+  krms1<<<4096, 128, 0, stream>>>(x, attnw, h1_hi, h1_lo, h1b, macc);
+  gemm_x3<2,2,2,2><<<dim3(64,1,1), 256, 0, stream>>>(h1_hi, h1_lo, wrT_hi, wrT_lo,
+      logits, 512, 512, 512, 64, 1.0f, 0,0,1, 0,0,1, 0,0,1);
+  krouter<<<1024, 256, 0, stream>>>(logits, probs, idx, wts, flagcnt, flaglist);
+  kfix<<<1024, 256, 0, stream>>>(flagcnt, flaglist, qkv, x, w_o, router_w, idx, wts, probs);
+  kcount<<<96, 256, 0, stream>>>(idx, cnt);
   ksump<<<64, 256, 0, stream>>>(probs, sumP);
   kfinalize<<<1, 64, 0, stream>>>(cnt, offs, tiles, ntl);
   kscatter<<<96, 256, 0, stream>>>(idx, wts, offs, cursor, rowsl, wrowl);
 
-  gemm_bf16<0><<<dim3(256, 24, 1), 256, 0, stream>>>(h1b, r_wgu, gu, nullptr,
+  kconvT<true><<<dim3(48,8,64), 256, 0, stream>>>(r_wgu, wguT, 512, 3072);
+  kconvT<true><<<dim3(48,8,2),  256, 0, stream>>>(s_wgu, sguT, 512, 3072);
+  gemm_ffn<0><<<dim3(256,24,1), 256, 0, stream>>>(h1b, wguT, hact, nullptr,
       offs, tiles, ntl, rowsl, wrowl, 3072, 512);
-  gemm_bf16<2><<<dim3(32, 24, 2), 256, 0, stream>>>(h1b, s_wgu, sgu, nullptr,
+  gemm_ffn<2><<<dim3(32,24,2), 256, 0, stream>>>(h1b, sguT, shact, nullptr,
       offs, tiles, ntl, rowsl, wrowl, 3072, 512);
-  kact<<<(24576*192 + 255)/256, 256, 0, stream>>>(gu, hact, 24576*192);
-  kact<<<(8192*192 + 255)/256, 256, 0, stream>>>(sgu, shact, 8192*192);
-  gemm_bf16<1><<<dim3(256, 4, 1), 256, 0, stream>>>(hact, r_wd, nullptr, macc,
+  kconvT<false><<<dim3(8,24,64), 256, 0, stream>>>(r_wd, wdT, 1536, 512);
+  kconvT<false><<<dim3(8,24,2),  256, 0, stream>>>(s_wd, swdT, 1536, 512);
+  gemm_ffn<1><<<dim3(256,4,1), 256, 0, stream>>>(hact, wdT, nullptr, macc,
       offs, tiles, ntl, rowsl, wrowl, 512, 1536);
-  gemm_bf16<3><<<dim3(32, 4, 2), 256, 0, stream>>>(shact, s_wd, nullptr, macc,
+  gemm_ffn<3><<<dim3(32,4,2), 256, 0, stream>>>(shact, swdT, nullptr, macc,
       offs, tiles, ntl, rowsl, wrowl, 512, 1536);
 
   krms2<<<4096, 128, 0, stream>>>(macc, out);
-  kscalars<<<1, 64, 0, stream>>>(cnt, sumP, out + 4096ULL*512);
-}
+  kscalars<<<1, 64, 0, stream>>>(cnt, sumP, out + 2097152);
+}
```

Result: slower. 2.201 ms (+99.5%).
